# Performance work log

Hardware: AMD Instinct MI355X
Metric: run time of the kernel (lower is better)

## Reference

```python
import jax, jax.numpy as jnp
import numpy as np

EPS = 1e-7  # keras.backend.epsilon()
CANONICAL_SIZE = 224.0
CANONICAL_LEVEL = 1.0
MIN_LEVEL, MAX_LEVEL = 0, 4


def _crop_and_resize(feat, boxes, crop_h, crop_w):
    """TF crop_and_resize (bilinear, extrapolation_value=0) for one image.
    feat: [H, W, C]; boxes: [N, 4] normalized (y1, x1, y2, x2).
    Returns [N, crop_h, crop_w, C]."""
    H, W, C = feat.shape
    hf = jnp.asarray(H - 1, feat.dtype)
    wf = jnp.asarray(W - 1, feat.dtype)
    y1, x1, y2, x2 = boxes[:, 0], boxes[:, 1], boxes[:, 2], boxes[:, 3]
    ty = jnp.arange(crop_h, dtype=feat.dtype) / (crop_h - 1)  # [ch]
    tx = jnp.arange(crop_w, dtype=feat.dtype) / (crop_w - 1)  # [cw]
    ys = (y1[:, None] + (y2 - y1)[:, None] * ty[None, :]) * hf  # [N, ch]
    xs = (x1[:, None] + (x2 - x1)[:, None] * tx[None, :]) * wf  # [N, cw]
    valid_y = (ys >= 0) & (ys <= hf)
    valid_x = (xs >= 0) & (xs <= wf)
    y0 = jnp.floor(ys)
    x0 = jnp.floor(xs)
    ly = ys - y0  # lerp weights [N, ch]
    lx = xs - x0  # [N, cw]
    y0i = jnp.clip(y0, 0, H - 1).astype(jnp.int32)
    y1i = jnp.clip(y0 + 1, 0, H - 1).astype(jnp.int32)
    x0i = jnp.clip(x0, 0, W - 1).astype(jnp.int32)
    x1i = jnp.clip(x0 + 1, 0, W - 1).astype(jnp.int32)
    # gather 4 corners -> [N, ch, cw, C]
    f00 = feat[y0i[:, :, None], x0i[:, None, :]]
    f01 = feat[y0i[:, :, None], x1i[:, None, :]]
    f10 = feat[y1i[:, :, None], x0i[:, None, :]]
    f11 = feat[y1i[:, :, None], x1i[:, None, :]]
    wy = ly[:, :, None, None]
    wx = lx[:, None, :, None]
    top = f00 + (f01 - f00) * wx
    bot = f10 + (f11 - f10) * wx
    out = top + (bot - top) * wy
    valid = (valid_y[:, :, None] & valid_x[:, None, :])[..., None]
    return jnp.where(valid, out, jnp.zeros((), feat.dtype))


def _map_to_level(boxes):
    w = boxes[:, 2] - boxes[:, 0]
    h = boxes[:, 3] - boxes[:, 1]
    size = jnp.sqrt(w * h)
    levels = jnp.floor(CANONICAL_LEVEL + jnp.log2(size / CANONICAL_SIZE + EPS))
    return jnp.clip(levels, MIN_LEVEL, MAX_LEVEL).astype(jnp.int32)


def roi_align(detections, fpn, top_k=1000, crop_size=(14, 14)):
    det = detections[0]                       # [N, 4+num_classes]
    scores = jnp.max(det[:, 4:], axis=1)      # [N]
    _, idx = jax.lax.top_k(scores, top_k)
    det = det[idx]                            # [K, 4+nc]
    levels = _map_to_level(det[:, :4])        # [K]
    # original concatenates level-0 rois, then level-1, ... == stable sort by level
    order = jnp.argsort(levels, stable=True)
    det = det[order]
    levels = levels[order]
    ch, cw = crop_size
    C = fpn[0].shape[-1]
    out = jnp.zeros((top_k, ch, cw, C), fpn[0].dtype)
    for i, f in enumerate(fpn):
        feat = f[0]                           # [H, W, C]
        H, W = feat.shape[0], feat.shape[1]
        hf = jnp.asarray(H - 1, feat.dtype)
        wf = jnp.asarray(W - 1, feat.dtype)
        boxes = jnp.stack([det[:, 1] / hf, det[:, 0] / wf,
                           det[:, 3] / hf, det[:, 2] / wf], axis=1)
        crops = _crop_and_resize(feat, boxes, ch, cw)
        out = jnp.where((levels == i)[:, None, None, None], crops, out)
    return out[None]                          # [1, K, ch, cw, C]


def setup_inputs() -> dict:
    key = jax.random.key(0)
    ks = jax.random.split(key, 10)
    N, NC = 5000, 80
    cx = jax.random.uniform(ks[0], (N,)) * 1024.0
    cy = jax.random.uniform(ks[1], (N,)) * 1024.0
    size = jnp.exp2(jax.random.uniform(ks[2], (N,)) * 5.0 + 5.0)   # 32..1024
    ar = jnp.exp2(jax.random.uniform(ks[3], (N,)) * 2.0 - 1.0)     # 0.5..2
    w = size * jnp.sqrt(ar)
    h = size / jnp.sqrt(ar)
    x1 = jnp.maximum(cx - w / 2, 0.0)
    y1 = jnp.maximum(cy - h / 2, 0.0)
    x2 = x1 + w
    y2 = y1 + h
    cls = jax.random.uniform(ks[4], (N, NC))
    detections = jnp.concatenate(
        [jnp.stack([x1, y1, x2, y2], axis=1), cls], axis=1)[None]  # [1,N,84]
    C = 256
    shapes = [256, 128, 64, 32, 16]
    fpn = {f"p{i}": jax.random.normal(ks[5 + i], (1, s, s, C), jnp.float32)
           for i, s in enumerate(shapes)}
    return {"detections": detections, **fpn}


def reference(detections, p0, p1, p2, p3, p4):
    return roi_align(detections, [p0, p1, p2, p3, p4],
                     top_k=1000, crop_size=(14, 14))
```

## Files before the change

### kernel.cpp

```cpp
#include <hip/hip_runtime.h>

#define NDET 5000
#define NCLS 80
#define DSTR 84
#define TOPK 1000
#define CROP 14
#define NPIX (CROP * CROP)
#define C    256

#define JCHUNK 250
#define ICHUNK 256

typedef float v4f __attribute__((ext_vector_type(4)));

__global__ void scores_kernel(const float* __restrict__ det, float* __restrict__ scores,
                              int* __restrict__ rank) {
    int i = blockIdx.x * blockDim.x + threadIdx.x;
    if (i >= NDET) return;
    const float* row = det + i * DSTR + 4;
    float m = row[0];
    #pragma unroll
    for (int c = 1; c < NCLS; ++c) m = fmaxf(m, row[c]);
    scores[i] = m;
    rank[i] = 0;
}

__global__ __launch_bounds__(ICHUNK) void rank_kernel(const float* __restrict__ scores,
                                                      int* __restrict__ rank) {
    __shared__ float s[JCHUNK];
    int jbase = blockIdx.y * JCHUNK;
    for (int t = threadIdx.x; t < JCHUNK; t += blockDim.x) s[t] = scores[jbase + t];
    __syncthreads();
    int i = blockIdx.x * ICHUNK + threadIdx.x;
    if (i >= NDET) return;
    float my = scores[i];
    int r = 0;
    #pragma unroll 5
    for (int t = 0; t < JCHUNK; ++t) {
        float v = s[t];
        int j = jbase + t;
        r += (v > my) | ((v == my) & (j < i));
    }
    atomicAdd(&rank[i], r);
}

__global__ void scatter_kernel(const int* __restrict__ rank, int* __restrict__ topk_idx) {
    int i = blockIdx.x * blockDim.x + threadIdx.x;
    if (i >= NDET) return;
    int r = rank[i];
    if (r < TOPK) topk_idx[r] = i;
}

__global__ __launch_bounds__(1024) void order_kernel(const float* __restrict__ det,
                                                     const int* __restrict__ topk_idx,
                                                     int* __restrict__ slot_det,
                                                     int* __restrict__ slot_level) {
    __shared__ unsigned long long wave_tot[16];
    int r = threadIdx.x;
    int di = 0, L = 0;
    unsigned long long key = 0;
    if (r < TOPK) {
        di = topk_idx[r];
        const float* b = det + di * DSTR;
        float w = b[2] - b[0];
        float h = b[3] - b[1];
        float sz = sqrtf(w * h);
        float lf = floorf(1.0f + log2f(sz / 224.0f + 1e-7f));
        lf = fminf(fmaxf(lf, 0.0f), 4.0f);
        L = (int)lf;
        key = 1ULL << (12 * L);
    }
    unsigned long long incl = key;
    #pragma unroll
    for (int d = 1; d < 64; d <<= 1) {
        unsigned long long up = __shfl_up(incl, d, 64);
        if ((r & 63) >= d) incl += up;
    }
    int wave = r >> 6;
    if ((r & 63) == 63) wave_tot[wave] = incl;
    __syncthreads();
    unsigned long long waveoff = 0, total = 0;
    for (int w = 0; w < 16; ++w) {
        unsigned long long t = wave_tot[w];
        if (w < wave) waveoff += t;
        total += t;
    }
    if (r < TOPK) {
        unsigned long long excl = waveoff + incl - key;
        int base = 0;
        for (int l = 0; l < L; ++l) base += (int)((total >> (12 * l)) & 0xFFF);
        int within = (int)((excl >> (12 * L)) & 0xFFF);
        int pos = base + within;
        slot_det[pos] = di;
        slot_level[pos] = L;
    }
}

__global__ __launch_bounds__(256) void crop_kernel(
    const float* __restrict__ det,
    const float* __restrict__ p0, const float* __restrict__ p1,
    const float* __restrict__ p2, const float* __restrict__ p3,
    const float* __restrict__ p4,
    const int* __restrict__ slot_det, const int* __restrict__ slot_level,
    float* __restrict__ out)
{
    int wave = threadIdx.x >> 6;
    int lane = threadIdx.x & 63;
    int slot = blockIdx.x >> 1;
    int sub  = blockIdx.x & 1;
    int wp   = sub * 4 + wave;

    int di = slot_det[slot];
    int L  = slot_level[slot];

    const float* feat; int H;
    switch (L) {
        case 0:  feat = p0; H = 256; break;
        case 1:  feat = p1; H = 128; break;
        case 2:  feat = p2; H = 64;  break;
        case 3:  feat = p3; H = 32;  break;
        default: feat = p4; H = 16;  break;
    }
    float hf = (float)(H - 1);

    const float* b = det + di * DSTR;
    float x1n = b[0] / hf, y1n = b[1] / hf;
    float x2n = b[2] / hf, y2n = b[3] / hf;
    float* outbase = out + (size_t)slot * NPIX * C;

    for (int p = wp; p < NPIX; p += 8) {
        int py = p / CROP;
        int px = p - py * CROP;
        float ty = (float)py / 13.0f;
        float tx = (float)px / 13.0f;
        float ys = (y1n + (y2n - y1n) * ty) * hf;
        float xs = (x1n + (x2n - x1n) * tx) * hf;

        v4f* outp = (v4f*)(outbase + (size_t)p * C) + lane;

        bool valid = (ys >= 0.0f) & (ys <= hf) & (xs >= 0.0f) & (xs <= hf);
        if (!valid) {
            v4f z = {0.0f, 0.0f, 0.0f, 0.0f};
            __builtin_nontemporal_store(z, outp);
            continue;
        }

        float y0f = floorf(ys), x0f = floorf(xs);
        float ly = ys - y0f,    lx = xs - x0f;
        int y0i = (int)fminf(fmaxf(y0f,        0.0f), hf);
        int y1i = (int)fminf(fmaxf(y0f + 1.0f, 0.0f), hf);
        int x0i = (int)fminf(fmaxf(x0f,        0.0f), hf);
        int x1i = (int)fminf(fmaxf(x0f + 1.0f, 0.0f), hf);

        v4f f00 = ((const v4f*)(feat + (size_t)(y0i * H + x0i) * C))[lane];
        v4f f01 = ((const v4f*)(feat + (size_t)(y0i * H + x1i) * C))[lane];
        v4f f10 = ((const v4f*)(feat + (size_t)(y1i * H + x0i) * C))[lane];
        v4f f11 = ((const v4f*)(feat + (size_t)(y1i * H + x1i) * C))[lane];

        v4f top = f00 + (f01 - f00) * lx;
        v4f bot = f10 + (f11 - f10) * lx;
        v4f o   = top + (bot - top) * ly;
        __builtin_nontemporal_store(o, outp);
    }
}

extern "C" void kernel_launch(void* const* d_in, const int* in_sizes, int n_in,
                              void* d_out, int out_size, void* d_ws, size_t ws_size,
                              hipStream_t stream) {
    const float* det = (const float*)d_in[0];
    const float* p0  = (const float*)d_in[1];
    const float* p1  = (const float*)d_in[2];
    const float* p2  = (const float*)d_in[3];
    const float* p3  = (const float*)d_in[4];
    const float* p4  = (const float*)d_in[5];
    float* out = (float*)d_out;

    char* ws = (char*)d_ws;
    float* scores    = (float*)(ws + 0);
    int*   rank      = (int*)(ws + 20000);
    int*   topk_idx  = (int*)(ws + 40000);
    int*   slot_det  = (int*)(ws + 44000);
    int*   slot_lvl  = (int*)(ws + 48000);

    scores_kernel<<<(NDET + 255) / 256, 256, 0, stream>>>(det, scores, rank);
    dim3 rg((NDET + ICHUNK - 1) / ICHUNK, NDET / JCHUNK);
    rank_kernel<<<rg, ICHUNK, 0, stream>>>(scores, rank);
    scatter_kernel<<<(NDET + 255) / 256, 256, 0, stream>>>(rank, topk_idx);
    order_kernel<<<1, 1024, 0, stream>>>(det, topk_idx, slot_det, slot_lvl);
    crop_kernel<<<TOPK * 2, 256, 0, stream>>>(det, p0, p1, p2, p3, p4,
                                              slot_det, slot_lvl, out);
}
```

Before: 305.1 us.

## Split crop into zero-fill plus compacted worklist of valid sample pixels

Output is first cleared by a dedicated zero kernel. A worklist kernel then computes validity for every (slot, pixel) pair and compacts the valid ones using ballot and atomics. A persistent gather kernel processes only those entries, doing the bilinear interpolation and plain stores. The aim is to skip wasted work on out-of-range pixels and balance load across waves. The cost is two extra launches, a full second write pass over the zero regions, and an extra worklist read.

Result: slower. 322.9 us (+5.8%).

```diff
diff --git a/kernel.cpp b/kernel.cpp
--- a/kernel.cpp
+++ b/kernel.cpp
@@ -7,15 +7,25 @@
 #define CROP 14
 #define NPIX (CROP * CROP)
 #define C    256
+#define NPAIR (TOPK * NPIX)
 
 #define JCHUNK 250
 #define ICHUNK 256
 
 typedef float v4f __attribute__((ext_vector_type(4)));
 
+__global__ __launch_bounds__(256) void zero_kernel(float* __restrict__ out) {
+    v4f* o = (v4f*)out;
+    int base = blockIdx.x * 2048 + threadIdx.x;
+    v4f z = {0.0f, 0.0f, 0.0f, 0.0f};
+    #pragma unroll
+    for (int k = 0; k < 8; ++k) o[base + k * 256] = z;
+}
+
 __global__ void scores_kernel(const float* __restrict__ det, float* __restrict__ scores,
-                              int* __restrict__ rank) {
+                              int* __restrict__ rank, int* __restrict__ counter) {
     int i = blockIdx.x * blockDim.x + threadIdx.x;
+    if (i == 0) *counter = 0;
     if (i >= NDET) return;
     const float* row = det + i * DSTR + 4;
     float m = row[0];
@@ -96,54 +106,84 @@
     }
 }
 
-__global__ __launch_bounds__(256) void crop_kernel(
+__device__ __forceinline__ void sample_coords(const float* __restrict__ b, float hf,
+                                              int py, int px, float& ys, float& xs) {
+    float x1n = b[0] / hf, y1n = b[1] / hf;
+    float x2n = b[2] / hf, y2n = b[3] / hf;
+    float ty = (float)py / 13.0f;
+    float tx = (float)px / 13.0f;
+    ys = (y1n + (y2n - y1n) * ty) * hf;
+    xs = (x1n + (x2n - x1n) * tx) * hf;
+}
+
+__device__ __forceinline__ int level_H(int L) {
+    return 256 >> L;
+}
+
+__global__ __launch_bounds__(256) void worklist_kernel(
+    const float* __restrict__ det,
+    const int* __restrict__ slot_det, const int* __restrict__ slot_level,
+    int* __restrict__ counter, int* __restrict__ worklist)
+{
+    int idx = blockIdx.x * blockDim.x + threadIdx.x;
+    int lane = threadIdx.x & 63;
+    bool valid = false;
+    int entry = 0;
+    if (idx < NPAIR) {
+        int s = idx / NPIX;
+        int p = idx - s * NPIX;
+        int py = p / CROP, px = p - py * CROP;
+        int L = slot_level[s];
+        int di = slot_det[s];
+        float hf = (float)(level_H(L) - 1);
+        float ys, xs;
+        sample_coords(det + di * DSTR, hf, py, px, ys, xs);
+        valid = (ys >= 0.0f) & (ys <= hf) & (xs >= 0.0f) & (xs <= hf);
+        entry = (s << 8) | p;
+    }
+    unsigned long long mask = __ballot(valid);
+    int myoff = __popcll(mask & ((1ULL << lane) - 1ULL));
+    int cnt = __popcll(mask);
+    int base = 0;
+    if (lane == 0) base = atomicAdd(counter, cnt);
+    base = __shfl(base, 0, 64);
+    if (valid) worklist[base + myoff] = entry;
+}
+
+#define GBLOCKS 1024
+#define GWAVES (GBLOCKS * 4)
+
+__global__ __launch_bounds__(256) void gather_kernel(
     const float* __restrict__ det,
     const float* __restrict__ p0, const float* __restrict__ p1,
     const float* __restrict__ p2, const float* __restrict__ p3,
     const float* __restrict__ p4,
     const int* __restrict__ slot_det, const int* __restrict__ slot_level,
+    const int* __restrict__ counter, const int* __restrict__ worklist,
     float* __restrict__ out)
 {
-    int wave = threadIdx.x >> 6;
     int lane = threadIdx.x & 63;
-    int slot = blockIdx.x >> 1;
-    int sub  = blockIdx.x & 1;
-    int wp   = sub * 4 + wave;
-
-    int di = slot_det[slot];
-    int L  = slot_level[slot];
-
-    const float* feat; int H;
-    switch (L) {
-        case 0:  feat = p0; H = 256; break;
-        case 1:  feat = p1; H = 128; break;
-        case 2:  feat = p2; H = 64;  break;
-        case 3:  feat = p3; H = 32;  break;
-        default: feat = p4; H = 16;  break;
-    }
-    float hf = (float)(H - 1);
-
-    const float* b = det + di * DSTR;
-    float x1n = b[0] / hf, y1n = b[1] / hf;
-    float x2n = b[2] / hf, y2n = b[3] / hf;
-    float* outbase = out + (size_t)slot * NPIX * C;
-
-    for (int p = wp; p < NPIX; p += 8) {
-        int py = p / CROP;
-        int px = p - py * CROP;
-        float ty = (float)py / 13.0f;
-        float tx = (float)px / 13.0f;
-        float ys = (y1n + (y2n - y1n) * ty) * hf;
-        float xs = (x1n + (x2n - x1n) * tx) * hf;
-
-        v4f* outp = (v4f*)(outbase + (size_t)p * C) + lane;
-
-        bool valid = (ys >= 0.0f) & (ys <= hf) & (xs >= 0.0f) & (xs <= hf);
-        if (!valid) {
-            v4f z = {0.0f, 0.0f, 0.0f, 0.0f};
-            __builtin_nontemporal_store(z, outp);
-            continue;
+    int w = blockIdx.x * 4 + (threadIdx.x >> 6);
+    int count = *counter;
+    for (int e = w; e < count; e += GWAVES) {
+        int ent = worklist[e];
+        int s = ent >> 8;
+        int p = ent & 255;
+        int py = p / CROP, px = p - py * CROP;
+        int di = slot_det[s];
+        int L  = slot_level[s];
+        const float* feat;
+        switch (L) {
+            case 0:  feat = p0; break;
+            case 1:  feat = p1; break;
+            case 2:  feat = p2; break;
+            case 3:  feat = p3; break;
+            default: feat = p4; break;
         }
+        int H = level_H(L);
+        float hf = (float)(H - 1);
+        float ys, xs;
+        sample_coords(det + di * DSTR, hf, py, px, ys, xs);
 
         float y0f = floorf(ys), x0f = floorf(xs);
         float ly = ys - y0f,    lx = xs - x0f;
@@ -160,7 +200,7 @@
         v4f top = f00 + (f01 - f00) * lx;
         v4f bot = f10 + (f11 - f10) * lx;
         v4f o   = top + (bot - top) * ly;
-        __builtin_nontemporal_store(o, outp);
+        ((v4f*)(out + (size_t)(s * NPIX + p) * C))[lane] = o;
     }
 }
 
@@ -181,12 +221,17 @@
     int*   topk_idx  = (int*)(ws + 40000);
     int*   slot_det  = (int*)(ws + 44000);
     int*   slot_lvl  = (int*)(ws + 48000);
-
-    scores_kernel<<<(NDET + 255) / 256, 256, 0, stream>>>(det, scores, rank);
+    int*   counter   = (int*)(ws + 52000);
+    int*   worklist  = (int*)(ws + 52096);
+
+    zero_kernel<<<6125, 256, 0, stream>>>(out);
+    scores_kernel<<<(NDET + 255) / 256, 256, 0, stream>>>(det, scores, rank, counter);
     dim3 rg((NDET + ICHUNK - 1) / ICHUNK, NDET / JCHUNK);
     rank_kernel<<<rg, ICHUNK, 0, stream>>>(scores, rank);
     scatter_kernel<<<(NDET + 255) / 256, 256, 0, stream>>>(rank, topk_idx);
     order_kernel<<<1, 1024, 0, stream>>>(det, topk_idx, slot_det, slot_lvl);
-    crop_kernel<<<TOPK * 2, 256, 0, stream>>>(det, p0, p1, p2, p3, p4,
-                                              slot_det, slot_lvl, out);
-}
+    worklist_kernel<<<(NPAIR + 255) / 256, 256, 0, stream>>>(det, slot_det, slot_lvl,
+                                                             counter, worklist);
+    gather_kernel<<<GBLOCKS, 256, 0, stream>>>(det, p0, p1, p2, p3, p4,
+                                               slot_det, slot_lvl, counter, worklist, out);
+}
```

## Fuse top-k scatter into order kernel and split crops across more blocks

Applied to the files above, without the earlier changes.

The top-k scatter kernel is folded into the single-block order kernel, which now builds the index table in shared memory, removing one launch and a global round trip. The crop kernel grid grows from two to thirteen blocks per ROI, each wave handling four consecutive pixels in an unrolled loop, to expose more parallelism and memory-level parallelism. Nontemporal output stores are replaced by ordinary stores. This adds more blocks with repeated per-ROI setup, leaves some waves idle in the last sub-block, and output now goes through the cache.

Measured after the change: 290.5 us. 1.05x faster.

```diff
diff --git a/kernel.cpp b/kernel.cpp
--- a/kernel.cpp
+++ b/kernel.cpp
@@ -44,23 +44,23 @@
     atomicAdd(&rank[i], r);
 }
 
-__global__ void scatter_kernel(const int* __restrict__ rank, int* __restrict__ topk_idx) {
-    int i = blockIdx.x * blockDim.x + threadIdx.x;
-    if (i >= NDET) return;
-    int r = rank[i];
-    if (r < TOPK) topk_idx[r] = i;
-}
-
 __global__ __launch_bounds__(1024) void order_kernel(const float* __restrict__ det,
-                                                     const int* __restrict__ topk_idx,
+                                                     const int* __restrict__ rank,
                                                      int* __restrict__ slot_det,
                                                      int* __restrict__ slot_level) {
+    __shared__ int topk_idx_s[TOPK];
     __shared__ unsigned long long wave_tot[16];
     int r = threadIdx.x;
+    for (int i = r; i < NDET; i += 1024) {
+        int rk = rank[i];
+        if (rk < TOPK) topk_idx_s[rk] = i;
+    }
+    __syncthreads();
+
     int di = 0, L = 0;
     unsigned long long key = 0;
     if (r < TOPK) {
-        di = topk_idx[r];
+        di = topk_idx_s[r];
         const float* b = det + di * DSTR;
         float w = b[2] - b[0];
         float h = b[3] - b[1];
@@ -106,9 +106,9 @@
 {
     int wave = threadIdx.x >> 6;
     int lane = threadIdx.x & 63;
-    int slot = blockIdx.x >> 1;
-    int sub  = blockIdx.x & 1;
-    int wp   = sub * 4 + wave;
+    int slot = blockIdx.x / 13;
+    int sub  = blockIdx.x % 13;
+    int pbase = sub * 16 + wave * 4;
 
     int di = slot_det[slot];
     int L  = slot_level[slot];
@@ -128,7 +128,10 @@
     float x2n = b[2] / hf, y2n = b[3] / hf;
     float* outbase = out + (size_t)slot * NPIX * C;
 
-    for (int p = wp; p < NPIX; p += 8) {
+    #pragma unroll
+    for (int j = 0; j < 4; ++j) {
+        int p = pbase + j;
+        if (p >= NPIX) break;
         int py = p / CROP;
         int px = p - py * CROP;
         float ty = (float)py / 13.0f;
@@ -141,7 +144,7 @@
         bool valid = (ys >= 0.0f) & (ys <= hf) & (xs >= 0.0f) & (xs <= hf);
         if (!valid) {
             v4f z = {0.0f, 0.0f, 0.0f, 0.0f};
-            __builtin_nontemporal_store(z, outp);
+            *outp = z;
             continue;
         }
 
@@ -160,7 +163,7 @@
         v4f top = f00 + (f01 - f00) * lx;
         v4f bot = f10 + (f11 - f10) * lx;
         v4f o   = top + (bot - top) * ly;
-        __builtin_nontemporal_store(o, outp);
+        *outp = o;
     }
 }
 
@@ -178,15 +181,13 @@
     char* ws = (char*)d_ws;
     float* scores    = (float*)(ws + 0);
     int*   rank      = (int*)(ws + 20000);
-    int*   topk_idx  = (int*)(ws + 40000);
-    int*   slot_det  = (int*)(ws + 44000);
-    int*   slot_lvl  = (int*)(ws + 48000);
+    int*   slot_det  = (int*)(ws + 40000);
+    int*   slot_lvl  = (int*)(ws + 44000);
 
     scores_kernel<<<(NDET + 255) / 256, 256, 0, stream>>>(det, scores, rank);
     dim3 rg((NDET + ICHUNK - 1) / ICHUNK, NDET / JCHUNK);
     rank_kernel<<<rg, ICHUNK, 0, stream>>>(scores, rank);
-    scatter_kernel<<<(NDET + 255) / 256, 256, 0, stream>>>(rank, topk_idx);
-    order_kernel<<<1, 1024, 0, stream>>>(det, topk_idx, slot_det, slot_lvl);
-    crop_kernel<<<TOPK * 2, 256, 0, stream>>>(det, p0, p1, p2, p3, p4,
-                                              slot_det, slot_lvl, out);
+    order_kernel<<<1, 1024, 0, stream>>>(det, rank, slot_det, slot_lvl);
+    crop_kernel<<<TOPK * 13, 256, 0, stream>>>(det, p0, p1, p2, p3, p4,
+                                               slot_det, slot_lvl, out);
 }
```
